# Optimization experiments

Measured on AMD Instinct MI355X. Metric: run time of the kernel, lower is better.

Reference implementation:

```python
import jax, jax.numpy as jnp
import numpy as np

N_NODES = 100000
N_EDGES = 1600000
N_GRAPHS = 512
F_IN = 20
HID = 128
OUT = HID // 2


def _glorot(key, shape):
    fan_in, fan_out = shape[0], shape[1]
    lim = float(np.sqrt(6.0 / (fan_in + fan_out)))
    return jax.random.uniform(key, shape, jnp.float32, -lim, lim)


def setup_inputs() -> dict:
    key = jax.random.key(0)
    ks = jax.random.split(key, 12)
    x = jax.random.normal(ks[0], (N_NODES, F_IN), jnp.float32)
    edge_index = jax.random.randint(ks[1], (2, N_EDGES), 0, N_NODES, dtype=jnp.int64)
    batch = jnp.sort(jax.random.randint(ks[2], (N_NODES,), 0, N_GRAPHS, dtype=jnp.int64))
    return {
        "x": x,
        "edge_index": edge_index,
        "batch": batch,
        "W1": _glorot(ks[3], (F_IN, HID)), "b1": jnp.zeros((HID,), jnp.float32),
        "W2": _glorot(ks[4], (HID, HID)), "b2": jnp.zeros((HID,), jnp.float32),
        "W3": _glorot(ks[5], (HID, HID)), "b3": jnp.zeros((HID,), jnp.float32),
        "Wout": _glorot(ks[6], (HID, OUT)), "bout": jnp.zeros((OUT,), jnp.float32),
    }


def _gcn_conv(x, W, b, src, dst, num_nodes):
    # PyG GCNConv: x' = D^{-1/2} (A + I) D^{-1/2} X W + b (self-loops already in src/dst)
    xw = x @ W                                                  # [N, H]
    ones = jnp.ones(src.shape[0], dtype=xw.dtype)
    deg = jax.ops.segment_sum(ones, dst, num_segments=num_nodes)
    dinv = jnp.where(deg > 0, jax.lax.rsqrt(deg), 0.0)          # [N]
    norm = dinv[src] * dinv[dst]                                # [E+N]
    msg = xw[src] * norm[:, None]                               # gather + scale
    return jax.ops.segment_sum(msg, dst, num_segments=num_nodes) + b


def reference(x, edge_index, batch, W1, b1, W2, b2, W3, b3, Wout, bout):
    num_nodes = x.shape[0]
    loops = jnp.arange(num_nodes, dtype=edge_index.dtype)
    src = jnp.concatenate([edge_index[0], loops])
    dst = jnp.concatenate([edge_index[1], loops])

    h = jax.nn.relu(_gcn_conv(x, W1, b1, src, dst, num_nodes))
    h = jax.nn.relu(_gcn_conv(h, W2, b2, src, dst, num_nodes))
    h = jax.nn.relu(_gcn_conv(h, W3, b3, src, dst, num_nodes))

    # global_mean_pool over graph ids
    sums = jax.ops.segment_sum(h, batch, num_segments=N_GRAPHS)
    counts = jax.ops.segment_sum(jnp.ones(num_nodes, h.dtype), batch, num_segments=N_GRAPHS)
    pooled = sums / jnp.maximum(counts, 1.0)[:, None]           # [G, H]
    return pooled @ Wout + bout                                 # [G, H//2]
```

## Files before the change

kernel.cpp:

```cpp
#include <hip/hip_runtime.h>
#include <hip/hip_fp16.h>

#define N_NODES 100000
#define N_EDGES 1600000
#define N_GRAPHS 512
#define F_IN 20
#define HID 128
#define OUT_F 64

#define BUCKETS 512
#define SPAN 196
#define BCAP 3500
#define EPB 4096

typedef _Float16 half8_t __attribute__((ext_vector_type(8)));
typedef float f32x4_t __attribute__((ext_vector_type(4)));
typedef unsigned int uv4 __attribute__((ext_vector_type(4)));

__device__ inline float4 h4_to_f4(uint2 u) {
    __half2 h0 = *(__half2*)&u.x;
    __half2 h1 = *(__half2*)&u.y;
    float2 f0 = __half22float2(h0);
    float2 f1 = __half22float2(h1);
    return make_float4(f0.x, f0.y, f1.x, f1.y);
}

__device__ inline float4 f4_from(unsigned a, unsigned b) {
    __half2 h0 = *(__half2*)&a;
    __half2 h1 = *(__half2*)&b;
    float2 f0 = __half22float2(h0);
    float2 f1 = __half22float2(h1);
    return make_float4(f0.x, f0.y, f1.x, f1.y);
}

__device__ inline void acc8(float4& aL, float4& aH, uv4 v) {
    float4 l_ = f4_from(v[0], v[1]);
    float4 h_ = f4_from(v[2], v[3]);
    aL.x += l_.x; aL.y += l_.y; aL.z += l_.z; aL.w += l_.w;
    aH.x += h_.x; aH.y += h_.y; aH.z += h_.z; aH.w += h_.w;
}

__global__ __launch_bounds__(512) void partition(const int* __restrict__ src,
                                                 const int* __restrict__ dst,
                                                 int* __restrict__ bpairs,
                                                 int* cur512) {
    __shared__ int lcnt[8][BUCKETS];
    __shared__ int woff[8][BUCKETS];
    __shared__ int loffx[BUCKETS];
    __shared__ int gbase[BUCKETS];
    __shared__ int sc[512];
    __shared__ int stage[EPB];
    __shared__ unsigned short sbuck[EPB];
    __shared__ int stot;
    int t = threadIdx.x;
    int wv = t >> 6;
    for (int i = t; i < 8 * BUCKETS; i += 512) ((int*)lcnt)[i] = 0;
    __syncthreads();
    int base = blockIdx.x * EPB;
    int myb[8], myp[8], myr[8];
#pragma unroll
    for (int i = 0; i < 8; ++i) {
        int e = base + i * 512 + t;
        int b = -1, p = 0, rk = 0;
        if (e < N_EDGES) {
            int s = src[e], d = dst[e];
            b = d / SPAN;
            p = (s << 9) | (d - b * SPAN);
            rk = atomicAdd(&lcnt[wv][b], 1);
        }
        myb[i] = b; myp[i] = p; myr[i] = rk;
    }
    __syncthreads();
    int c[8], tot = 0;
#pragma unroll
    for (int w = 0; w < 8; ++w) { c[w] = lcnt[w][t]; tot += c[w]; }
    sc[t] = tot;
    __syncthreads();
    for (int o = 1; o < BUCKETS; o <<= 1) {
        int v = (t >= o) ? sc[t - o] : 0;
        __syncthreads();
        sc[t] += v;
        __syncthreads();
    }
    int excl = sc[t] - tot;
    loffx[t] = excl;
    gbase[t] = atomicAdd(&cur512[t], tot);
    {
        int lb = excl;
#pragma unroll
        for (int w = 0; w < 8; ++w) { woff[w][t] = lb; lb += c[w]; }
    }
    if (t == 511) stot = sc[511];
    __syncthreads();
#pragma unroll
    for (int i = 0; i < 8; ++i) {
        int b = myb[i];
        if (b >= 0) {
            int slot = woff[wv][b] + myr[i];
            stage[slot] = myp[i];
            sbuck[slot] = (unsigned short)b;
        }
    }
    __syncthreads();
    int n = stot;
    for (int i = t; i < n; i += 512) {
        int b = sbuck[i];
        int pos = gbase[b] + (i - loffx[b]);
        if (pos < BCAP) bpairs[(size_t)b * BCAP + pos] = stage[i];
    }
}

__global__ __launch_bounds__(512) void csr_build(const int* __restrict__ bpairs,
                                                 const int* __restrict__ cur512,
                                                 int* __restrict__ row_st,
                                                 int* __restrict__ csr,
                                                 const float* __restrict__ x,
                                                 __half* __restrict__ Xs) {
    __shared__ int ocnt[SPAN];
    __shared__ int sc[512];
    __shared__ int cur[SPAN];
    __shared__ int lcsr[BCAP];
    __shared__ int sbase;
    int b = blockIdx.x, t = threadIdx.x;

    int myc = cur512[t];
    sc[t] = myc;
    __syncthreads();
    for (int o = 1; o < BUCKETS; o <<= 1) {
        int v = (t >= o) ? sc[t - o] : 0;
        __syncthreads();
        sc[t] += v;
        __syncthreads();
    }
    if (t == b) sbase = sc[t] - myc;
    if (b == BUCKETS - 1 && t == 0) row_st[N_NODES] = N_EDGES;

    int n0 = b * SPAN;
    int span = N_NODES - n0; if (span > SPAN) span = SPAN;
    if (span < 0) span = 0;
    if (t < SPAN) ocnt[t] = 0;
    __syncthreads();

    int n = cur512[b];
    if (n > BCAP) n = BCAP;
    const int* p = bpairs + (size_t)b * BCAP;
    for (int i = t; i < n; i += 512) atomicAdd(&ocnt[p[i] & 511], 1);
    __syncthreads();
    sc[t] = (t < span) ? ocnt[t] : 0;
    __syncthreads();
    for (int o = 1; o < 512; o <<= 1) {
        int v = (t >= o) ? sc[t - o] : 0;
        __syncthreads();
        sc[t] += v;
        __syncthreads();
    }
    int base = sbase;
    if (t < span) {
        int start = sc[t] - ocnt[t];
        row_st[n0 + t] = base + start;
        cur[t] = start;
    }
    __syncthreads();
    for (int i = t; i < n; i += 512) {
        int e = p[i];
        int lp = atomicAdd(&cur[e & 511], 1);
        lcsr[lp] = e >> 9;
    }
    __syncthreads();
    for (int i = t; i < n; i += 512)
        csr[base + i] = lcsr[i];
    for (int i = t; i < span * 32; i += 512) {
        int nl = i >> 5, f = i & 31;
        float v = (f < F_IN) ? x[(size_t)(n0 + nl) * F_IN + f] : 0.f;
        float di = rsqrtf((float)(ocnt[nl] + 1));
        Xs[(size_t)(n0 + nl) * 32 + f] = __float2half(di * v);
    }
}

__global__ __launch_bounds__(256) void gather20(const __half* __restrict__ Xs,
                                                const int* __restrict__ row_st,
                                                const int* __restrict__ csr,
                                                float* __restrict__ A20) {
    const int t = threadIdx.x;
    const int n = blockIdx.x * 64 + (t >> 2);
    const int l = t & 3;
    if (n >= N_NODES) return;
    int r0 = row_st[n], r1 = row_st[n + 1];
    const uv4* X4 = (const uv4*)Xs;
    uv4 u = X4[(size_t)n * 4 + l];
    float4 accL = f4_from(u[0], u[1]);
    float4 accH = f4_from(u[2], u[3]);
    int r = r0;
    for (; r + 7 < r1; r += 8) {
        int s0 = csr[r],     s1 = csr[r + 1], s2 = csr[r + 2], s3 = csr[r + 3];
        int s4 = csr[r + 4], s5 = csr[r + 5], s6 = csr[r + 6], s7 = csr[r + 7];
        uv4 vv0 = X4[(size_t)s0 * 4 + l];
        uv4 vv1 = X4[(size_t)s1 * 4 + l];
        uv4 vv2 = X4[(size_t)s2 * 4 + l];
        uv4 vv3 = X4[(size_t)s3 * 4 + l];
        uv4 vv4 = X4[(size_t)s4 * 4 + l];
        uv4 vv5 = X4[(size_t)s5 * 4 + l];
        uv4 vv6 = X4[(size_t)s6 * 4 + l];
        uv4 vv7 = X4[(size_t)s7 * 4 + l];
        uv4 vv[8] = {vv0, vv1, vv2, vv3, vv4, vv5, vv6, vv7};
#pragma unroll
        for (int j = 0; j < 8; ++j) acc8(accL, accH, vv[j]);
    }
    for (; r < r1; ++r) acc8(accL, accH, X4[(size_t)csr[r] * 4 + l]);
    float di = rsqrtf((float)(r1 - r0 + 1));
    accL.x *= di; accL.y *= di; accL.z *= di; accL.w *= di;
    accH.x *= di; accH.y *= di; accH.z *= di; accH.w *= di;
    float4* ap = (float4*)(A20 + (size_t)n * 32 + l * 8);
    ap[0] = accL;
    ap[1] = accH;
}

__global__ __launch_bounds__(256) void gemm20(const float* __restrict__ A20,
                                              const float* __restrict__ W,
                                              const float* __restrict__ bias,
                                              __half* __restrict__ H) {
    __shared__ float Wlds[F_IN * HID];
    __shared__ float Alds[64][F_IN];
    const int t = threadIdx.x;
    const int node0 = blockIdx.x * 64;

    for (int i = t; i < F_IN * HID; i += 256) Wlds[i] = W[i];
    for (int i = t; i < 64 * 32; i += 256) {
        int nl = i >> 5, f = i & 31;
        if (f < F_IN && node0 + nl < N_NODES)
            Alds[nl][f] = A20[(size_t)(node0 + nl) * 32 + f];
    }
    __syncthreads();

    const int nl = t >> 2;
    const int cb = (t & 3) * 4;
    float4 acc[8];
#pragma unroll
    for (int j = 0; j < 8; ++j) acc[j] = *(const float4*)&bias[cb + 16 * j];
#pragma unroll
    for (int k = 0; k < F_IN; ++k) {
        float a = Alds[nl][k];
        const float* Wr = &Wlds[k * HID + cb];
#pragma unroll
        for (int j = 0; j < 8; ++j) {
            float4 w = *(const float4*)&Wr[16 * j];
            acc[j].x = fmaf(a, w.x, acc[j].x);
            acc[j].y = fmaf(a, w.y, acc[j].y);
            acc[j].z = fmaf(a, w.z, acc[j].z);
            acc[j].w = fmaf(a, w.w, acc[j].w);
        }
    }
    if (node0 + nl < N_NODES) {
#pragma unroll
        for (int j = 0; j < 8; ++j) {
            int c = cb + 16 * j;
            int slice = c >> 6;
            int wi = ((c & 63) >> 2);
            __half2 h0 = __floats2half2_rn(acc[j].x, acc[j].y);
            __half2 h1 = __floats2half2_rn(acc[j].z, acc[j].w);
            uint2 u; u.x = *(unsigned*)&h0; u.y = *(unsigned*)&h1;
            ((uint2*)H)[((size_t)slice * N_NODES + node0 + nl) * 16 + wi] = u;
        }
    }
}

__global__ __launch_bounds__(256) void gemm_mfma(const __half* __restrict__ H,
                                                 const float* __restrict__ W,
                                                 const int* __restrict__ row_st,
                                                 __half* __restrict__ T) {
    __shared__ _Float16 Whi[64 * 128];
    __shared__ _Float16 Wlo[64 * 128];
    const int t = threadIdx.x;
    const int c0 = (blockIdx.x & 1) * 64;

    for (int i = t; i < 128 * 64; i += 256) {
        int k = i >> 6, c = i & 63;
        float w = W[k * HID + c0 + c];
        _Float16 hi = (_Float16)w;
        _Float16 lo = (_Float16)((w - (float)hi) * 2048.0f);
        int addr = c * 128 + (((k >> 3) ^ (c & 15)) << 3) + (k & 7);
        Whi[addr] = hi;
        Wlo[addr] = lo;
    }
    __syncthreads();

    const int wv = t >> 6;
    const int l  = t & 63;
    const int lr = l & 15;
    const int lq = l >> 4;

    for (int rep = 0; rep < 4; ++rep) {
        int strip = ((blockIdx.x >> 1) * 4 + wv) * 4 + rep;
        if (strip >= N_NODES / 16) continue;
        int n0 = strip * 16;

        f32x4_t acc[4], acl[4];
#pragma unroll
        for (int ct = 0; ct < 4; ++ct) { acc[ct] = (f32x4_t){0,0,0,0}; acl[ct] = (f32x4_t){0,0,0,0}; }

#pragma unroll
        for (int kc = 0; kc < 4; ++kc) {
            half8_t a = *(const half8_t*)(H + ((size_t)(kc >> 1) * N_NODES + n0 + lr) * 64
                                            + (kc & 1) * 32 + lq * 8);
#pragma unroll
            for (int j = 0; j < 8; ++j) a[j] = a[j] > (_Float16)0 ? a[j] : (_Float16)0;
            int g = kc * 4 + lq;
#pragma unroll
            for (int ct = 0; ct < 4; ++ct) {
                int c = ct * 16 + lr;
                int addr = c * 128 + ((g ^ lr) << 3);
                half8_t bh = *(const half8_t*)&Whi[addr];
                half8_t bl = *(const half8_t*)&Wlo[addr];
                acc[ct] = __builtin_amdgcn_mfma_f32_16x16x32_f16(a, bh, acc[ct], 0, 0, 0);
                acl[ct] = __builtin_amdgcn_mfma_f32_16x16x32_f16(a, bl, acl[ct], 0, 0, 0);
            }
        }

        int r0 = n0 + lq * 4;
#pragma unroll
        for (int r = 0; r < 4; ++r) {
            int row = r0 + r;
            float d = rsqrtf((float)(row_st[row + 1] - row_st[row] + 1));
#pragma unroll
            for (int ct = 0; ct < 4; ++ct) {
                float v = (acc[ct][r] + acl[ct][r] * 4.8828125e-4f) * d;
                int c = c0 + ct * 16 + lr;
                T[((size_t)(c >> 6) * N_NODES + row) * 64 + (c & 63)] = __float2half(v);
            }
        }
    }
}

__global__ __launch_bounds__(256) void gather_half(const __half* __restrict__ T,
                                                   const int* __restrict__ row_st,
                                                   const int* __restrict__ csr,
                                                   const float* __restrict__ bias,
                                                   __half* __restrict__ B) {
    int t = threadIdx.x;
    int b = blockIdx.x;
    int x = b & 7;
    int slice = x >> 2;
    int chunk = (b >> 3) * 4 + (x & 3);
    int n = chunk * 32 + (t >> 3);
    int l = t & 7;
    if (n >= N_NODES) return;
    int r0 = row_st[n], r1 = row_st[n + 1];
    float di = rsqrtf((float)(r1 - r0 + 1));
    const uv4* Tf = (const uv4*)T + (size_t)slice * N_NODES * 8;
    uv4 u = Tf[(size_t)n * 8 + l];
    float4 accL = f4_from(u[0], u[1]);
    float4 accH = f4_from(u[2], u[3]);
    int r = r0;
    for (; r + 7 < r1; r += 8) {
        int s0 = csr[r],     s1 = csr[r + 1], s2 = csr[r + 2], s3 = csr[r + 3];
        int s4 = csr[r + 4], s5 = csr[r + 5], s6 = csr[r + 6], s7 = csr[r + 7];
        uv4 vv0 = Tf[(size_t)s0 * 8 + l];
        uv4 vv1 = Tf[(size_t)s1 * 8 + l];
        uv4 vv2 = Tf[(size_t)s2 * 8 + l];
        uv4 vv3 = Tf[(size_t)s3 * 8 + l];
        uv4 vv4 = Tf[(size_t)s4 * 8 + l];
        uv4 vv5 = Tf[(size_t)s5 * 8 + l];
        uv4 vv6 = Tf[(size_t)s6 * 8 + l];
        uv4 vv7 = Tf[(size_t)s7 * 8 + l];
        uv4 vv[8] = {vv0, vv1, vv2, vv3, vv4, vv5, vv6, vv7};
#pragma unroll
        for (int j = 0; j < 8; ++j) {
            float4 aL = f4_from(vv[j][0], vv[j][1]);
            float4 aH = f4_from(vv[j][2], vv[j][3]);
            accL.x += aL.x; accL.y += aL.y; accL.z += aL.z; accL.w += aL.w;
            accH.x += aH.x; accH.y += aH.y; accH.z += aH.z; accH.w += aH.w;
        }
    }
    for (; r + 3 < r1; r += 4) {
        int s0 = csr[r], s1 = csr[r + 1], s2 = csr[r + 2], s3 = csr[r + 3];
        uv4 vv0 = Tf[(size_t)s0 * 8 + l];
        uv4 vv1 = Tf[(size_t)s1 * 8 + l];
        uv4 vv2 = Tf[(size_t)s2 * 8 + l];
        uv4 vv3 = Tf[(size_t)s3 * 8 + l];
        uv4 vv[4] = {vv0, vv1, vv2, vv3};
#pragma unroll
        for (int j = 0; j < 4; ++j) {
            float4 aL = f4_from(vv[j][0], vv[j][1]);
            float4 aH = f4_from(vv[j][2], vv[j][3]);
            accL.x += aL.x; accL.y += aL.y; accL.z += aL.z; accL.w += aL.w;
            accH.x += aH.x; accH.y += aH.y; accH.z += aH.z; accH.w += aH.w;
        }
    }
    for (; r < r1; ++r) {
        uv4 v = Tf[(size_t)csr[r] * 8 + l];
        float4 aL = f4_from(v[0], v[1]);
        float4 aH = f4_from(v[2], v[3]);
        accL.x += aL.x; accL.y += aL.y; accL.z += aL.z; accL.w += aL.w;
        accH.x += aH.x; accH.y += aH.y; accH.z += aH.z; accH.w += aH.w;
    }
    const float4* bb = (const float4*)bias + slice * 16 + l * 2;
    float4 b0 = bb[0], b1 = bb[1];
    __half2 h0 = __floats2half2_rn(fmaf(di, accL.x, b0.x), fmaf(di, accL.y, b0.y));
    __half2 h1 = __floats2half2_rn(fmaf(di, accL.z, b0.z), fmaf(di, accL.w, b0.w));
    __half2 h2 = __floats2half2_rn(fmaf(di, accH.x, b1.x), fmaf(di, accH.y, b1.y));
    __half2 h3 = __floats2half2_rn(fmaf(di, accH.z, b1.z), fmaf(di, accH.w, b1.w));
    uv4 o;
    o[0] = *(unsigned*)&h0; o[1] = *(unsigned*)&h1;
    o[2] = *(unsigned*)&h2; o[3] = *(unsigned*)&h3;
    uv4* dstp = (uv4*)B + ((size_t)slice * N_NODES + n) * 8 + l;
    __builtin_nontemporal_store(o, dstp);
}

__global__ __launch_bounds__(256) void pool_head(const __half* __restrict__ H,
                                                 const int* __restrict__ batch,
                                                 const float* __restrict__ Wout,
                                                 const float* __restrict__ bout,
                                                 float* __restrict__ out) {
    __shared__ float4 part[8][32];
    __shared__ float p[HID];
    __shared__ int bounds[2];
    int g = blockIdx.x;
    int t = threadIdx.x;
    if (t < 2) {
        int target = g + t;
        int lo = 0, hi = N_NODES;
        while (lo < hi) {
            int mid = (lo + hi) >> 1;
            if (batch[mid] < target) lo = mid + 1; else hi = mid;
        }
        bounds[t] = lo;
    }
    __syncthreads();
    int lo = bounds[0], hi = bounds[1];
    int grp = t >> 5, l = t & 31;
    const uint2* Hf = (const uint2*)H;
    float4 acc = make_float4(0.f, 0.f, 0.f, 0.f);
    const size_t sbase = (size_t)(l >> 4) * N_NODES;
    const int wi = l & 15;
    for (int n = lo + grp; n < hi; n += 8) {
        float4 v = h4_to_f4(Hf[(sbase + n) * 16 + wi]);
        acc.x += fmaxf(v.x, 0.f);
        acc.y += fmaxf(v.y, 0.f);
        acc.z += fmaxf(v.z, 0.f);
        acc.w += fmaxf(v.w, 0.f);
    }
    part[grp][l] = acc;
    __syncthreads();
    if (t < 32) {
        float4 s = part[0][t];
#pragma unroll
        for (int j = 1; j < 8; ++j) {
            float4 v = part[j][t];
            s.x += v.x; s.y += v.y; s.z += v.z; s.w += v.w;
        }
        float inv = 1.0f / fmaxf((float)(hi - lo), 1.0f);
        p[t * 4 + 0] = s.x * inv;
        p[t * 4 + 1] = s.y * inv;
        p[t * 4 + 2] = s.z * inv;
        p[t * 4 + 3] = s.w * inv;
    }
    __syncthreads();
    if (t < OUT_F) {
        float acc2 = 0.f;
#pragma unroll 8
        for (int k = 0; k < HID; ++k)
            acc2 = fmaf(p[k], Wout[k * OUT_F + t], acc2);
        out[g * OUT_F + t] = acc2 + bout[t];
    }
}

extern "C" void kernel_launch(void* const* d_in, const int* in_sizes, int n_in,
                              void* d_out, int out_size, void* d_ws, size_t ws_size,
                              hipStream_t stream) {
    const float* x     = (const float*)d_in[0];
    const int*   ei    = (const int*)d_in[1];
    const int*   batch = (const int*)d_in[2];
    const float* W1    = (const float*)d_in[3];
    const float* b1    = (const float*)d_in[4];
    const float* W2    = (const float*)d_in[5];
    const float* b2    = (const float*)d_in[6];
    const float* W3    = (const float*)d_in[7];
    const float* b3    = (const float*)d_in[8];
    const float* Wout  = (const float*)d_in[9];
    const float* bout  = (const float*)d_in[10];
    float* out = (float*)d_out;

    const int* src = ei;
    const int* dst = ei + N_EDGES;

    float* A      = (float*)d_ws;
    float* Breg   = A + (size_t)N_NODES * HID;
    int*   row_st = (int*)(Breg + (size_t)N_NODES * HID);
    int*   cur512 = row_st + N_NODES + 1;
    int*   csr    = cur512 + BUCKETS;

    int*    bpairs = (int*)A;
    __half* Xs     = (__half*)((char*)A + 7168000);
    __half* T      = (__half*)A;
    __half* H      = (__half*)Breg;
    float*  A20    = (float*)((char*)A + 26u * 1024 * 1024);

    hipMemsetAsync(cur512, 0, BUCKETS * sizeof(int), stream);
    partition<<<(N_EDGES + EPB - 1) / EPB, 512, 0, stream>>>(src, dst, bpairs, cur512);
    csr_build<<<BUCKETS, 512, 0, stream>>>(bpairs, cur512, row_st, csr, x, Xs);

    gather20<<<(N_NODES + 63) / 64, 256, 0, stream>>>(Xs, row_st, csr, A20);
    gemm20<<<(N_NODES + 63) / 64, 256, 0, stream>>>(A20, W1, b1, H);

    gemm_mfma<<<782, 256, 0, stream>>>(H, W2, row_st, T);
    gather_half<<<6256, 256, 0, stream>>>(T, row_st, csr, b2, H);
    gemm_mfma<<<782, 256, 0, stream>>>(H, W3, row_st, T);
    gather_half<<<6256, 256, 0, stream>>>(T, row_st, csr, b3, H);

    pool_head<<<N_GRAPHS, 256, 0, stream>>>(H, batch, Wout, bout, out);
}
```

Measured before the change: 343.6 us.

## Fuse layer-1 small GEMM with layer-2 MFMA transform into one kernel

Replaces the separate gemm20 kernel (A20·W1+b1 → fp16 H in global memory) and the first gemm_mfma with a single kernel. Each wave computes the ReLU'd layer-1 activations for a 16-node strip in registers and stages them in swizzled LDS. It then runs the split-precision fp16 MFMA against W2 and scales rows by the degree normalisation. This removes one launch and the global round trip of the 100k×128 H tensor. The cost is that the 20×128 layer-1 product is recomputed in both column-half blocks, and the layer-1 result now stays in fp16 inside LDS.

```diff
diff --git a/kernel.cpp b/kernel.cpp
--- a/kernel.cpp
+++ b/kernel.cpp
@@ -215,51 +215,102 @@
     ap[1] = accH;
 }
 
-__global__ __launch_bounds__(256) void gemm20(const float* __restrict__ A20,
-                                              const float* __restrict__ W,
-                                              const float* __restrict__ bias,
-                                              __half* __restrict__ H) {
-    __shared__ float Wlds[F_IN * HID];
-    __shared__ float Alds[64][F_IN];
+__global__ __launch_bounds__(256) void gemm_l1(const float* __restrict__ A20,
+                                               const float* __restrict__ W1,
+                                               const float* __restrict__ b1,
+                                               const float* __restrict__ W2,
+                                               const int* __restrict__ row_st,
+                                               __half* __restrict__ T) {
+    __shared__ _Float16 Whi[64 * 128];
+    __shared__ _Float16 Wlo[64 * 128];
+    __shared__ float W1s[F_IN * HID];
+    __shared__ __align__(16) _Float16 Hs[4][16 * 128];
     const int t = threadIdx.x;
-    const int node0 = blockIdx.x * 64;
-
-    for (int i = t; i < F_IN * HID; i += 256) Wlds[i] = W[i];
-    for (int i = t; i < 64 * 32; i += 256) {
-        int nl = i >> 5, f = i & 31;
-        if (f < F_IN && node0 + nl < N_NODES)
-            Alds[nl][f] = A20[(size_t)(node0 + nl) * 32 + f];
-    }
-    __syncthreads();
-
-    const int nl = t >> 2;
-    const int cb = (t & 3) * 4;
-    float4 acc[8];
-#pragma unroll
-    for (int j = 0; j < 8; ++j) acc[j] = *(const float4*)&bias[cb + 16 * j];
-#pragma unroll
-    for (int k = 0; k < F_IN; ++k) {
-        float a = Alds[nl][k];
-        const float* Wr = &Wlds[k * HID + cb];
-#pragma unroll
-        for (int j = 0; j < 8; ++j) {
-            float4 w = *(const float4*)&Wr[16 * j];
-            acc[j].x = fmaf(a, w.x, acc[j].x);
-            acc[j].y = fmaf(a, w.y, acc[j].y);
-            acc[j].z = fmaf(a, w.z, acc[j].z);
-            acc[j].w = fmaf(a, w.w, acc[j].w);
-        }
-    }
-    if (node0 + nl < N_NODES) {
-#pragma unroll
-        for (int j = 0; j < 8; ++j) {
-            int c = cb + 16 * j;
-            int slice = c >> 6;
-            int wi = ((c & 63) >> 2);
-            __half2 h0 = __floats2half2_rn(acc[j].x, acc[j].y);
-            __half2 h1 = __floats2half2_rn(acc[j].z, acc[j].w);
-            uint2 u; u.x = *(unsigned*)&h0; u.y = *(unsigned*)&h1;
-            ((uint2*)H)[((size_t)slice * N_NODES + node0 + nl) * 16 + wi] = u;
+    const int c0 = (blockIdx.x & 1) * 64;
+
+    for (int i = t; i < 128 * 64; i += 256) {
+        int k = i >> 6, c = i & 63;
+        float w = W2[k * HID + c0 + c];
+        _Float16 hi = (_Float16)w;
+        _Float16 lo = (_Float16)((w - (float)hi) * 2048.0f);
+        int addr = c * 128 + (((k >> 3) ^ (c & 15)) << 3) + (k & 7);
+        Whi[addr] = hi;
+        Wlo[addr] = lo;
+    }
+    for (int i = t; i < F_IN * HID; i += 256) W1s[i] = W1[i];
+    __syncthreads();
+
+    const int wv = t >> 6;
+    const int ln = t & 63;
+    const int lr = ln & 15;
+    const int lq = ln >> 4;
+    char* myrow = (char*)&Hs[wv][0] + lr * 256;
+    const int sw = (lr & 7) << 4;
+
+    for (int rep = 0; rep < 4; ++rep) {
+        int strip = ((blockIdx.x >> 1) * 4 + wv) * 4 + rep;
+        if (strip >= N_NODES / 16) continue;
+        int n0 = strip * 16;
+
+        {
+            float a[F_IN];
+            const float* ar = A20 + (size_t)(n0 + lr) * 32;
+#pragma unroll
+            for (int k = 0; k < F_IN; ++k) a[k] = ar[k];
+            const int cb = lq * 32;
+#pragma unroll
+            for (int q = 0; q < 4; ++q) {
+                float v[8];
+#pragma unroll
+                for (int j = 0; j < 8; ++j) v[j] = b1[cb + q * 8 + j];
+#pragma unroll
+                for (int k = 0; k < F_IN; ++k) {
+                    float av = a[k];
+                    const float* wr = &W1s[k * HID + cb + q * 8];
+#pragma unroll
+                    for (int j = 0; j < 8; ++j) v[j] = fmaf(av, wr[j], v[j]);
+                }
+                __half2 h0 = __floats2half2_rn(fmaxf(v[0], 0.f), fmaxf(v[1], 0.f));
+                __half2 h1 = __floats2half2_rn(fmaxf(v[2], 0.f), fmaxf(v[3], 0.f));
+                __half2 h2 = __floats2half2_rn(fmaxf(v[4], 0.f), fmaxf(v[5], 0.f));
+                __half2 h3 = __floats2half2_rn(fmaxf(v[6], 0.f), fmaxf(v[7], 0.f));
+                uv4 u;
+                u[0] = *(unsigned*)&h0; u[1] = *(unsigned*)&h1;
+                u[2] = *(unsigned*)&h2; u[3] = *(unsigned*)&h3;
+                *(uv4*)(myrow + ((lq * 64 + q * 16) ^ sw)) = u;
+            }
+        }
+        asm volatile("s_waitcnt lgkmcnt(0)" ::: "memory");
+
+        f32x4_t acc[4], acl[4];
+#pragma unroll
+        for (int ct = 0; ct < 4; ++ct) { acc[ct] = (f32x4_t){0,0,0,0}; acl[ct] = (f32x4_t){0,0,0,0}; }
+#pragma unroll
+        for (int kc = 0; kc < 4; ++kc) {
+            half8_t a = *(const half8_t*)(myrow + ((kc * 64 + lq * 16) ^ sw));
+            int g = kc * 4 + lq;
+#pragma unroll
+            for (int ct = 0; ct < 4; ++ct) {
+                int c = ct * 16 + lr;
+                int addr = c * 128 + ((g ^ lr) << 3);
+                half8_t bh = *(const half8_t*)&Whi[addr];
+                half8_t bl = *(const half8_t*)&Wlo[addr];
+                acc[ct] = __builtin_amdgcn_mfma_f32_16x16x32_f16(a, bh, acc[ct], 0, 0, 0);
+                acl[ct] = __builtin_amdgcn_mfma_f32_16x16x32_f16(a, bl, acl[ct], 0, 0, 0);
+            }
+        }
+
+        int r0 = n0 + lq * 4;
+#pragma unroll
+        for (int r = 0; r < 4; ++r) {
+            int row = r0 + r;
+            float d = rsqrtf((float)(row_st[row + 1] - row_st[row] + 1));
+#pragma unroll
+            for (int ct = 0; ct < 4; ++ct) {
+                float v = (acc[ct][r] + acl[ct][r] * 4.8828125e-4f) * d;
+                int c = c0 + ct * 16 + lr;
+                T[((size_t)(c >> 6) * N_NODES + row) * 64 + (c & 63)] = __float2half(v);
+            }
         }
     }
 }
@@ -500,9 +551,9 @@
     csr_build<<<BUCKETS, 512, 0, stream>>>(bpairs, cur512, row_st, csr, x, Xs);
 
     gather20<<<(N_NODES + 63) / 64, 256, 0, stream>>>(Xs, row_st, csr, A20);
-    gemm20<<<(N_NODES + 63) / 64, 256, 0, stream>>>(A20, W1, b1, H);
-
-    gemm_mfma<<<782, 256, 0, stream>>>(H, W2, row_st, T);
+
+    gemm_l1<<<782, 256, 0, stream>>>(A20, W1, b1, W2, row_st, T);
+
     gather_half<<<6256, 256, 0, stream>>>(T, row_st, csr, b2, H);
     gemm_mfma<<<782, 256, 0, stream>>>(H, W3, row_st, T);
     gather_half<<<6256, 256, 0, stream>>>(T, row_st, csr, b3, H);
```

After: 356.6 us. +3.8%, slower.
